# Performance work log

Hardware: AMD Instinct MI355X
Metric: run time of the kernel (lower is better)

The kernel has to match this reference:

```python
import jax, jax.numpy as jnp
import numpy as np

GRID_NUM = 3  # pykan 'grid' (number of intervals)
K = 3         # spline order

def bspline_basis(x, grid, k):
    # Cox-de Boor recursion, matching pykan B_batch with a shared extended grid.
    # x: (N, Din); grid: (G,) extended grid with G = GRID_NUM + 2*k + 1
    x = x[..., None]  # (N, Din, 1)
    B = ((x >= grid[:-1]) & (x < grid[1:])).astype(x.dtype)  # (N, Din, G-1)
    for p in range(1, k + 1):
        left = (x - grid[:-(p + 1)]) / (grid[p:-1] - grid[:-(p + 1)])
        right = (grid[p + 1:] - x) / (grid[p + 1:] - grid[1:-p])
        B = left * B[..., :-1] + right * B[..., 1:]
    return B  # (N, Din, GRID_NUM + k)

def setup_inputs() -> dict:
    key = jax.random.key(0)
    k1, k2, k3 = jax.random.split(key, 3)
    Bsz, S, Din, Dout = 4, 2048, 768, 768
    x = jax.random.normal(k1, (Bsz, S, Din), dtype=jnp.float32)
    # noise-scale-like init for spline coefficients (noise_scale=0.1)
    coef = (0.1 / GRID_NUM) * jax.random.normal(k2, (Dout, Din, GRID_NUM + K), dtype=jnp.float32)
    inv_sqrt_in = np.float32(1.0 / np.sqrt(Din))
    scale_base = inv_sqrt_in + 0.1 * inv_sqrt_in * jax.random.normal(k3, (Dout, Din), dtype=jnp.float32)
    scale_sp = jnp.ones((Dout, Din), dtype=jnp.float32)
    bias = jnp.zeros((Dout,), dtype=jnp.float32)
    return {"x": x, "coef": coef, "scale_base": scale_base, "scale_sp": scale_sp, "bias": bias}

def reference(x, coef, scale_base, scale_sp, bias):
    # x: (B, S, Din) -> flatten tokens as the original module does
    Bsz, S, Din = x.shape
    xf = x.reshape(-1, Din)  # (N, Din)
    # extended grid: linspace(-1,1,GRID_NUM+1) extended by K points each side (h = 2/GRID_NUM)
    h = 2.0 / GRID_NUM
    grid = jnp.arange(-K, GRID_NUM + K + 1, dtype=x.dtype) * h - 1.0  # (GRID_NUM + 2K + 1,)
    basis = bspline_basis(xf, grid, K)  # (N, Din, GRID_NUM+K)
    # per-edge activation: scale_base*silu(x) + scale_sp*spline(x); mask==1; symbolic branch==0
    base = jax.nn.silu(xf) @ scale_base.T  # (N, Dout)
    spline = jnp.einsum('nim,oim->no', basis, scale_sp[:, :, None] * coef)  # (N, Dout)
    out = base + spline + bias  # bias from pykan biases[l].weight
    return out.reshape(Bsz, S, -1)
```

## Files before the change

kernel.cpp:

```cpp
#include <hip/hip_runtime.h>


typedef _Float16 f16;
typedef __attribute__((ext_vector_type(2))) _Float16 f16x2;
typedef __attribute__((ext_vector_type(4))) _Float16 f16x4;
typedef __attribute__((ext_vector_type(8))) _Float16 f16x8;
typedef __attribute__((ext_vector_type(4))) float f32x4;

#define NTOK 8192
#define DIN 768
#define DOUT 768
#define KAUG 5376
#define BM 128
#define BN 192
#define BK 64
#define NKT (KAUG / BK)
#define ASZ (BM * BK)
#define BSZ (BN * BK)
#define NBLK ((NTOK / BM) * (DOUT / BN))

typedef __attribute__((address_space(1))) void gvoid;
typedef __attribute__((address_space(3))) void lvoid;

__device__ __forceinline__ void spline6(float xv, float* __restrict__ B, float& s) {
  s = xv / (1.0f + __expf(-xv));
  const float h = 2.0f / 3.0f;
  float Bb[9];
#pragma unroll
  for (int g = 0; g < 9; ++g) {
    float t0 = (float)(g - 3) * h - 1.0f;
    float t1 = (float)(g - 2) * h - 1.0f;
    Bb[g] = (xv >= t0 && xv < t1) ? 1.0f : 0.0f;
  }
#pragma unroll
  for (int p = 1; p <= 3; ++p) {
    float inv = 1.0f / ((float)p * h);
#pragma unroll
    for (int j = 0; j < 8; ++j) {
      if (j < 9 - p) {
        float tj = (float)(j - 3) * h - 1.0f;
        float tjp1 = (float)(j + p + 1 - 3) * h - 1.0f;
        Bb[j] = (xv - tj) * inv * Bb[j] + (tjp1 - xv) * inv * Bb[j + 1];
      }
    }
  }
#pragma unroll
  for (int m = 0; m < 6; ++m) B[m] = Bb[m];
}

#define NBLK_A ((NTOK * DIN) / 1024)
#define NBLK_W ((DOUT * DIN) / 512)

__global__ __launch_bounds__(256) void build_AW(const float* __restrict__ x,
                                                const float* __restrict__ sb,
                                                const float* __restrict__ ssp,
                                                const float* __restrict__ coef,
                                                f16* __restrict__ Aa,
                                                f16* __restrict__ Wa) {
  const int b = blockIdx.x;
  if (b < NBLK_A) {
    int idx = (b * 256 + threadIdx.x) * 4;
    float4 xv = *(const float4*)(x + idx);
    int n = idx / DIN;
    int i = idx - n * DIN;

    float B0[6], B1[6], B2[6], B3[6];
    float s0, s1, s2, s3;
    spline6(xv.x, B0, s0);
    spline6(xv.y, B1, s1);
    spline6(xv.z, B2, s2);
    spline6(xv.w, B3, s3);

    size_t base = (size_t)n * KAUG + i;
    f16x4 sv = {(f16)s0, (f16)s1, (f16)s2, (f16)s3};
    *(f16x4*)(Aa + base) = sv;
#pragma unroll
    for (int m = 0; m < 6; ++m) {
      f16x4 bv = {(f16)B0[m], (f16)B1[m], (f16)B2[m], (f16)B3[m]};
      *(f16x4*)(Aa + base + (size_t)(m + 1) * DIN) = bv;
    }
  } else {
    int idx2 = ((b - NBLK_A) * 256 + threadIdx.x) * 2;
    float2 bb = *(const float2*)(sb + idx2);
    float2 pp = *(const float2*)(ssp + idx2);
    int o = idx2 / DIN;
    int i = idx2 - o * DIN;
    size_t base = (size_t)o * KAUG + i;
    f16x2 w0 = {(f16)bb.x, (f16)bb.y};
    *(f16x2*)(Wa + base) = w0;
    float4 c0 = *(const float4*)(coef + (size_t)idx2 * 6);
    float4 c1 = *(const float4*)(coef + (size_t)idx2 * 6 + 4);
    float4 c2 = *(const float4*)(coef + (size_t)idx2 * 6 + 8);
    float ma[6] = {c0.x, c0.y, c0.z, c0.w, c1.x, c1.y};
    float mb[6] = {c1.z, c1.w, c2.x, c2.y, c2.z, c2.w};
#pragma unroll
    for (int m = 0; m < 6; ++m) {
      f16x2 wv = {(f16)(pp.x * ma[m]), (f16)(pp.y * mb[m])};
      *(f16x2*)(Wa + base + (size_t)(m + 1) * DIN) = wv;
    }
  }
}

__global__ __launch_bounds__(512, 2) void kan_gemm(const f16* __restrict__ A,
                                                   const f16* __restrict__ W,
                                                   const float* __restrict__ bias,
                                                   float* __restrict__ out) {
  __shared__ alignas(16) f16 As[3 * ASZ];
  __shared__ alignas(16) f16 Bs[3 * BSZ];

  const int tid = threadIdx.x;
  const int wave = tid >> 6;
  const int lane = tid & 63;

  const int bid = blockIdx.x;
  const int wg = (bid & 7) * (NBLK / 8) + (bid >> 3);
  const int m0 = (wg >> 2) * BM;
  const int n0 = (wg & 3) * BN;

  const int wm = (wave >> 2) * 64;
  const int wn = (wave & 3) * 48;
  const int r = lane & 15;
  const int q = lane >> 4;
  const int r7 = r & 7;

  f32x4 acc[4][3] = {};

  const int cA0 = tid, cA1 = tid + 512;
  const int cB0 = tid, cB1 = tid + 512, cB2 = tid + 1024;
  const f16* gA0 = A + (size_t)(m0 + (cA0 >> 3)) * KAUG + ((cA0 & 7) ^ ((cA0 >> 3) & 7)) * 8;
  const f16* gA1 = A + (size_t)(m0 + (cA1 >> 3)) * KAUG + ((cA1 & 7) ^ ((cA1 >> 3) & 7)) * 8;
  const f16* gB0 = W + (size_t)(n0 + (cB0 >> 3)) * KAUG + ((cB0 & 7) ^ ((cB0 >> 3) & 7)) * 8;
  const f16* gB1 = W + (size_t)(n0 + (cB1 >> 3)) * KAUG + ((cB1 & 7) ^ ((cB1 >> 3) & 7)) * 8;
  const f16* gB2 = W + (size_t)(n0 + (cB2 >> 3)) * KAUG + ((cB2 & 7) ^ ((cB2 >> 3) & 7)) * 8;
  const int dA0 = wave * 512, dA1 = 4096 + wave * 512;
  const int dB0 = wave * 512, dB1 = 4096 + wave * 512, dB2 = 8192 + wave * 512;

#define STAGE_B(bufi, kt)                                                                  \
  do {                                                                                     \
    const int ko = (kt)*BK;                                                                \
    f16* bb_ = Bs + (bufi)*BSZ;                                                            \
    __builtin_amdgcn_global_load_lds((gvoid*)(gB0 + ko), (lvoid*)(bb_ + dB0), 16, 0, 0);   \
    __builtin_amdgcn_global_load_lds((gvoid*)(gB1 + ko), (lvoid*)(bb_ + dB1), 16, 0, 0);   \
    __builtin_amdgcn_global_load_lds((gvoid*)(gB2 + ko), (lvoid*)(bb_ + dB2), 16, 0, 0);   \
  } while (0)

#define STAGE_A(bufi, kt)                                                                  \
  do {                                                                                     \
    const int ko = (kt)*BK;                                                                \
    f16* ab_ = As + (bufi)*ASZ;                                                            \
    __builtin_amdgcn_global_load_lds((gvoid*)(gA0 + ko), (lvoid*)(ab_ + dA0), 16, 0, 0);   \
    __builtin_amdgcn_global_load_lds((gvoid*)(gA1 + ko), (lvoid*)(ab_ + dA1), 16, 0, 0);   \
  } while (0)

#define PH(bufi, kh, STAGE_STMT)                                                           \
  do {                                                                                     \
    const f16* Ab = As + (bufi)*ASZ;                                                       \
    const f16* Bb = Bs + (bufi)*BSZ;                                                       \
    const int sl = (((kh)*4 + q) ^ r7) * 8;                                                \
    f16x8 af[4], bf[3];                                                                    \
    _Pragma("unroll") for (int mi = 0; mi < 4; ++mi) af[mi] =                              \
        *(const f16x8*)&Ab[(wm + mi * 16 + r) * BK + sl];                                  \
    _Pragma("unroll") for (int ni = 0; ni < 3; ++ni) bf[ni] =                              \
        *(const f16x8*)&Bb[(wn + ni * 16 + r) * BK + sl];                                  \
    STAGE_STMT;                                                                            \
    __builtin_amdgcn_s_setprio(1);                                                         \
    _Pragma("unroll") for (int mi = 0; mi < 4; ++mi)                                       \
        _Pragma("unroll") for (int ni = 0; ni < 3; ++ni) acc[mi][ni] =                     \
        __builtin_amdgcn_mfma_f32_16x16x32_f16(af[mi], bf[ni], acc[mi][ni], 0, 0, 0);      \
    __builtin_amdgcn_s_setprio(0);                                                         \
  } while (0)

#define FENCE_BAR(VMC)                                            \
  do {                                                            \
    asm volatile("s_waitcnt lgkmcnt(0) vmcnt(" #VMC ")" ::: "memory"); \
    __builtin_amdgcn_sched_barrier(0);                            \
    __builtin_amdgcn_s_barrier();                                 \
  } while (0)

#define MID_BAR()                                                 \
  do {                                                            \
    asm volatile("s_waitcnt lgkmcnt(0)" ::: "memory");            \
    __builtin_amdgcn_sched_barrier(0);                            \
    __builtin_amdgcn_s_barrier();                                 \
  } while (0)

  STAGE_B(0, 0);
  STAGE_A(0, 0);
  STAGE_B(1, 1);
  STAGE_A(1, 1);
  FENCE_BAR(5);

  for (int t = 0; t < NKT - 2; ++t) {
    const int rb = t % 3;
    const int pb = (t + 2) % 3;
    PH(rb, 0, STAGE_B(pb, t + 2));
    MID_BAR();
    PH(rb, 1, STAGE_A(pb, t + 2));
    FENCE_BAR(5);
  }
  {
    const int rb = (NKT - 2) % 3;
    PH(rb, 0, (void)0);
    MID_BAR();
    PH(rb, 1, (void)0);
    FENCE_BAR(0);
  }
  {
    const int rb = (NKT - 1) % 3;
    PH(rb, 0, (void)0);
    PH(rb, 1, (void)0);
  }

#undef STAGE_A
#undef STAGE_B
#undef PH
#undef FENCE_BAR
#undef MID_BAR

#pragma unroll
  for (int mi = 0; mi < 4; ++mi) {
#pragma unroll
    for (int ni = 0; ni < 3; ++ni) {
      const int gcol = n0 + wn + ni * 16 + r;
      const float bv = bias[gcol];
#pragma unroll
      for (int rg = 0; rg < 4; ++rg) {
        const int grow = m0 + wm + mi * 16 + q * 4 + rg;
        out[(size_t)grow * DOUT + gcol] = acc[mi][ni][rg] + bv;
      }
    }
  }
}

extern "C" void kernel_launch(void* const* d_in, const int* in_sizes, int n_in,
                              void* d_out, int out_size, void* d_ws, size_t ws_size,
                              hipStream_t stream) {
  const float* x = (const float*)d_in[0];
  const float* coef = (const float*)d_in[1];
  const float* scale_base = (const float*)d_in[2];
  const float* scale_sp = (const float*)d_in[3];
  const float* bias = (const float*)d_in[4];
  float* out = (float*)d_out;

  f16* Aa = (f16*)d_ws;
  f16* Wa = (f16*)((char*)d_ws + (size_t)NTOK * KAUG * 2);

  build_AW<<<NBLK_A + NBLK_W, 256, 0, stream>>>(x, scale_base, scale_sp, coef, Aa, Wa);
  kan_gemm<<<NBLK, 512, 0, stream>>>(Aa, Wa, bias, out);
}
```

Before: 190.5 us.

## Use split-K with larger 256x192 tiles and atomic accumulation into bias-initialized output

```diff
diff --git a/kernel.cpp b/kernel.cpp
--- a/kernel.cpp
+++ b/kernel.cpp
@@ -11,13 +11,13 @@
 #define DIN 768
 #define DOUT 768
 #define KAUG 5376
-#define BM 128
+#define BM 256
 #define BN 192
 #define BK 64
-#define NKT (KAUG / BK)
+#define KHALF (KAUG / 2)
+#define NT (KHALF / BK)
 #define ASZ (BM * BK)
 #define BSZ (BN * BK)
-#define NBLK ((NTOK / BM) * (DOUT / BN))
 
 typedef __attribute__((address_space(1))) void gvoid;
 typedef __attribute__((address_space(3))) void lvoid;
@@ -101,11 +101,16 @@
   }
 }
 
+__global__ __launch_bounds__(256) void out_init(const float* __restrict__ bias,
+                                                float* __restrict__ out) {
+  int idx = blockIdx.x * 256 + threadIdx.x;
+  ((float4*)out)[idx] = ((const float4*)bias)[idx % (DOUT / 4)];
+}
+
 __global__ __launch_bounds__(512, 2) void kan_gemm(const f16* __restrict__ A,
                                                    const f16* __restrict__ W,
-                                                   const float* __restrict__ bias,
                                                    float* __restrict__ out) {
-  __shared__ alignas(16) f16 As[3 * ASZ];
+  __shared__ alignas(16) f16 As[2 * ASZ];
   __shared__ alignas(16) f16 Bs[3 * BSZ];
 
   const int tid = threadIdx.x;
@@ -113,68 +118,67 @@
   const int lane = tid & 63;
 
   const int bid = blockIdx.x;
-  const int wg = (bid & 7) * (NBLK / 8) + (bid >> 3);
-  const int m0 = (wg >> 2) * BM;
-  const int n0 = (wg & 3) * BN;
-
-  const int wm = (wave >> 2) * 64;
-  const int wn = (wave & 3) * 48;
+  const int xcd = bid & 7;
+  const int wg = xcd * 32 + (bid >> 3);
+  const int half = wg >> 7;
+  const int rem = wg & 127;
+  const int m0 = (rem >> 2) * BM;
+  const int n0 = (rem & 3) * BN;
+  const size_t k0 = (size_t)half * KHALF;
+
+  const int wm = (wave >> 1) * 64;
+  const int wn = (wave & 1) * 96;
   const int r = lane & 15;
   const int q = lane >> 4;
   const int r7 = r & 7;
 
-  f32x4 acc[4][3] = {};
-
-  const int cA0 = tid, cA1 = tid + 512;
-  const int cB0 = tid, cB1 = tid + 512, cB2 = tid + 1024;
-  const f16* gA0 = A + (size_t)(m0 + (cA0 >> 3)) * KAUG + ((cA0 & 7) ^ ((cA0 >> 3) & 7)) * 8;
-  const f16* gA1 = A + (size_t)(m0 + (cA1 >> 3)) * KAUG + ((cA1 & 7) ^ ((cA1 >> 3) & 7)) * 8;
-  const f16* gB0 = W + (size_t)(n0 + (cB0 >> 3)) * KAUG + ((cB0 & 7) ^ ((cB0 >> 3) & 7)) * 8;
-  const f16* gB1 = W + (size_t)(n0 + (cB1 >> 3)) * KAUG + ((cB1 & 7) ^ ((cB1 >> 3) & 7)) * 8;
-  const f16* gB2 = W + (size_t)(n0 + (cB2 >> 3)) * KAUG + ((cB2 & 7) ^ ((cB2 >> 3) & 7)) * 8;
-  const int dA0 = wave * 512, dA1 = 4096 + wave * 512;
-  const int dB0 = wave * 512, dB1 = 4096 + wave * 512, dB2 = 8192 + wave * 512;
-
-#define STAGE_B(bufi, kt)                                                                  \
-  do {                                                                                     \
-    const int ko = (kt)*BK;                                                                \
-    f16* bb_ = Bs + (bufi)*BSZ;                                                            \
-    __builtin_amdgcn_global_load_lds((gvoid*)(gB0 + ko), (lvoid*)(bb_ + dB0), 16, 0, 0);   \
-    __builtin_amdgcn_global_load_lds((gvoid*)(gB1 + ko), (lvoid*)(bb_ + dB1), 16, 0, 0);   \
-    __builtin_amdgcn_global_load_lds((gvoid*)(gB2 + ko), (lvoid*)(bb_ + dB2), 16, 0, 0);   \
-  } while (0)
-
-#define STAGE_A(bufi, kt)                                                                  \
-  do {                                                                                     \
-    const int ko = (kt)*BK;                                                                \
-    f16* ab_ = As + (bufi)*ASZ;                                                            \
-    __builtin_amdgcn_global_load_lds((gvoid*)(gA0 + ko), (lvoid*)(ab_ + dA0), 16, 0, 0);   \
-    __builtin_amdgcn_global_load_lds((gvoid*)(gA1 + ko), (lvoid*)(ab_ + dA1), 16, 0, 0);   \
-  } while (0)
-
-#define PH(bufi, kh, STAGE_STMT)                                                           \
-  do {                                                                                     \
-    const f16* Ab = As + (bufi)*ASZ;                                                       \
-    const f16* Bb = Bs + (bufi)*BSZ;                                                       \
-    const int sl = (((kh)*4 + q) ^ r7) * 8;                                                \
-    f16x8 af[4], bf[3];                                                                    \
-    _Pragma("unroll") for (int mi = 0; mi < 4; ++mi) af[mi] =                              \
-        *(const f16x8*)&Ab[(wm + mi * 16 + r) * BK + sl];                                  \
-    _Pragma("unroll") for (int ni = 0; ni < 3; ++ni) bf[ni] =                              \
-        *(const f16x8*)&Bb[(wn + ni * 16 + r) * BK + sl];                                  \
-    STAGE_STMT;                                                                            \
-    __builtin_amdgcn_s_setprio(1);                                                         \
-    _Pragma("unroll") for (int mi = 0; mi < 4; ++mi)                                       \
-        _Pragma("unroll") for (int ni = 0; ni < 3; ++ni) acc[mi][ni] =                     \
-        __builtin_amdgcn_mfma_f32_16x16x32_f16(af[mi], bf[ni], acc[mi][ni], 0, 0, 0);      \
-    __builtin_amdgcn_s_setprio(0);                                                         \
-  } while (0)
-
-#define FENCE_BAR(VMC)                                            \
-  do {                                                            \
-    asm volatile("s_waitcnt lgkmcnt(0) vmcnt(" #VMC ")" ::: "memory"); \
-    __builtin_amdgcn_sched_barrier(0);                            \
-    __builtin_amdgcn_s_barrier();                                 \
+  f32x4 acc[4][6] = {};
+
+  const f16* gA[4];
+  const f16* gB[3];
+#pragma unroll
+  for (int j = 0; j < 4; ++j) {
+    const int c = tid + j * 512;
+    gA[j] = A + (size_t)(m0 + (c >> 3)) * KAUG + k0 + (((c & 7) ^ ((c >> 3) & 7)) * 8);
+  }
+#pragma unroll
+  for (int j = 0; j < 3; ++j) {
+    const int c = tid + j * 512;
+    gB[j] = W + (size_t)(n0 + (c >> 3)) * KAUG + k0 + (((c & 7) ^ ((c >> 3) & 7)) * 8);
+  }
+
+#define STAGE_A(bufi, kt)                                                              \
+  do {                                                                                 \
+    const int ko = (kt)*BK;                                                            \
+    f16* ab_ = As + (bufi)*ASZ + wave * 512;                                           \
+    _Pragma("unroll") for (int j = 0; j < 4; ++j)                                      \
+        __builtin_amdgcn_global_load_lds((gvoid*)(gA[j] + ko),                         \
+                                         (lvoid*)(ab_ + j * 4096), 16, 0, 0);          \
+  } while (0)
+
+#define STAGE_B(bufi, kt)                                                              \
+  do {                                                                                 \
+    const int ko = (kt)*BK;                                                            \
+    f16* bb_ = Bs + (bufi)*BSZ + wave * 512;                                           \
+    _Pragma("unroll") for (int j = 0; j < 3; ++j)                                      \
+        __builtin_amdgcn_global_load_lds((gvoid*)(gB[j] + ko),                         \
+                                         (lvoid*)(bb_ + j * 4096), 16, 0, 0);          \
+  } while (0)
+
+#define PH(Ab, Bb, kh, STAGE_STMT)                                                     \
+  do {                                                                                 \
+    const int sl = (((kh)*4 + q) ^ r7) * 8;                                            \
+    f16x8 af[4], bf[6];                                                                \
+    _Pragma("unroll") for (int mi = 0; mi < 4; ++mi) af[mi] =                          \
+        *(const f16x8*)&(Ab)[(wm + mi * 16 + r) * BK + sl];                            \
+    _Pragma("unroll") for (int ni = 0; ni < 6; ++ni) bf[ni] =                          \
+        *(const f16x8*)&(Bb)[(wn + ni * 16 + r) * BK + sl];                            \
+    STAGE_STMT;                                                                        \
+    __builtin_amdgcn_s_setprio(1);                                                     \
+    _Pragma("unroll") for (int mi = 0; mi < 4; ++mi)                                   \
+        _Pragma("unroll") for (int ni = 0; ni < 6; ++ni) acc[mi][ni] =                 \
+        __builtin_amdgcn_mfma_f32_16x16x32_f16(af[mi], bf[ni], acc[mi][ni], 0, 0, 0);  \
+    __builtin_amdgcn_s_setprio(0);                                                     \
   } while (0)
 
 #define MID_BAR()                                                 \
@@ -184,49 +188,57 @@
     __builtin_amdgcn_s_barrier();                                 \
   } while (0)
 
+#define FENCE_BAR(VMC)                                                 \
+  do {                                                                 \
+    asm volatile("s_waitcnt lgkmcnt(0) vmcnt(" #VMC ")" ::: "memory"); \
+    __builtin_amdgcn_sched_barrier(0);                                 \
+    __builtin_amdgcn_s_barrier();                                      \
+  } while (0)
+
+  STAGE_A(0, 0);
   STAGE_B(0, 0);
-  STAGE_A(0, 0);
   STAGE_B(1, 1);
-  STAGE_A(1, 1);
-  FENCE_BAR(5);
-
-  for (int t = 0; t < NKT - 2; ++t) {
-    const int rb = t % 3;
-    const int pb = (t + 2) % 3;
-    PH(rb, 0, STAGE_B(pb, t + 2));
+  asm volatile("s_waitcnt vmcnt(3)" ::: "memory");
+  __builtin_amdgcn_sched_barrier(0);
+  __builtin_amdgcn_s_barrier();
+
+  for (int t = 0; t < NT; ++t) {
+    const f16* Ab = As + (t & 1) * ASZ;
+    const f16* Bb = Bs + (t % 3) * BSZ;
+
+    if (t + 1 < NT) {
+      PH(Ab, Bb, 0, STAGE_A((t + 1) & 1, t + 1));
+    } else {
+      PH(Ab, Bb, 0, (void)0);
+    }
     MID_BAR();
-    PH(rb, 1, STAGE_A(pb, t + 2));
-    FENCE_BAR(5);
-  }
-  {
-    const int rb = (NKT - 2) % 3;
-    PH(rb, 0, (void)0);
-    MID_BAR();
-    PH(rb, 1, (void)0);
-    FENCE_BAR(0);
-  }
-  {
-    const int rb = (NKT - 1) % 3;
-    PH(rb, 0, (void)0);
-    PH(rb, 1, (void)0);
+
+    if (t + 2 < NT) {
+      PH(Ab, Bb, 1, STAGE_B((t + 2) % 3, t + 2));
+      FENCE_BAR(3);
+    } else if (t + 1 < NT) {
+      PH(Ab, Bb, 1, (void)0);
+      FENCE_BAR(0);
+    } else {
+      PH(Ab, Bb, 1, (void)0);
+    }
   }
 
 #undef STAGE_A
 #undef STAGE_B
 #undef PH
+#undef MID_BAR
 #undef FENCE_BAR
-#undef MID_BAR
 
 #pragma unroll
   for (int mi = 0; mi < 4; ++mi) {
 #pragma unroll
-    for (int ni = 0; ni < 3; ++ni) {
+    for (int ni = 0; ni < 6; ++ni) {
       const int gcol = n0 + wn + ni * 16 + r;
-      const float bv = bias[gcol];
 #pragma unroll
       for (int rg = 0; rg < 4; ++rg) {
         const int grow = m0 + wm + mi * 16 + q * 4 + rg;
-        out[(size_t)grow * DOUT + gcol] = acc[mi][ni][rg] + bv;
+        unsafeAtomicAdd(&out[(size_t)grow * DOUT + gcol], acc[mi][ni][rg]);
       }
     }
   }
@@ -246,5 +258,6 @@
   f16* Wa = (f16*)((char*)d_ws + (size_t)NTOK * KAUG * 2);
 
   build_AW<<<NBLK_A + NBLK_W, 256, 0, stream>>>(x, scale_base, scale_sp, coef, Aa, Wa);
-  kan_gemm<<<NBLK, 512, 0, stream>>>(Aa, Wa, bias, out);
-}
+  out_init<<<(NTOK * DOUT / 4) / 256, 256, 0, stream>>>(bias, out);
+  kan_gemm<<<256, 512, 0, stream>>>(Aa, Wa, out);
+}
```

Result: slower. 208.0 us (+9.2%).
